# Optimization experiments

Hardware: AMD Instinct MI355X
Metric: run time of the kernel (lower is better)

The kernel has to match this reference:

```python
import jax, jax.numpy as jnp
import numpy as np
from functools import partial

S, E, K = 50000, 20000, 128
B = 16384
NE = 1000000
L = 2  # num_layer


def setup_inputs() -> dict:
    key = jax.random.key(0)
    ks = jax.random.split(key, 24)
    inp = {
        'stu_id': jax.random.randint(ks[0], (B,), 0, S),
        'input_exercise': jax.random.randint(ks[1], (B,), 0, E),
        'input_knowledge_point': jax.random.uniform(ks[2], (B, K), jnp.float32),
        'rows_1': jax.random.randint(ks[3], (NE,), 0, S),
        'cols_1': jax.random.randint(ks[4], (NE,), 0, E),
        'rows_0': jax.random.randint(ks[5], (NE,), 0, S),
        'cols_0': jax.random.randint(ks[6], (NE,), 0, E),
        'vals_ui_1': jax.random.uniform(ks[7], (NE,), jnp.float32),
        'vals_iu_1': jax.random.uniform(ks[8], (NE,), jnp.float32),
        'vals_ui_0': jax.random.uniform(ks[9], (NE,), jnp.float32),
        'vals_iu_0': jax.random.uniform(ks[10], (NE,), jnp.float32),
        'd_i_1': jax.random.uniform(ks[11], (S,), jnp.float32),
        'd_j_1': jax.random.uniform(ks[12], (E,), jnp.float32),
        'd_i_0': jax.random.uniform(ks[13], (S,), jnp.float32),
        'd_j_0': jax.random.uniform(ks[14], (E,), jnp.float32),
        'student_emb': jax.random.normal(ks[15], (S, K), jnp.float32) * 0.1,
        'exercise_emb': jax.random.normal(ks[16], (E, K), jnp.float32) * 0.1,
        'student_emb_bias': jax.random.normal(ks[17], (S, 1), jnp.float32) * 0.1,
        'e_discrimination': jax.random.normal(ks[18], (E, 1), jnp.float32) * 0.1,
        'W1': jax.random.normal(ks[19], (256, K), jnp.float32) * (1.0 / np.sqrt(K)),
        'b1': jnp.zeros((256,), jnp.float32),
        'W2': jax.random.normal(ks[20], (128, 256), jnp.float32) * (1.0 / np.sqrt(256)),
        'b2': jnp.zeros((128,), jnp.float32),
        'W3': jax.random.normal(ks[21], (1, 128), jnp.float32) * (1.0 / np.sqrt(128)),
        'b3': jnp.zeros((1,), jnp.float32),
    }
    return inp


def pos_linear(x, W, b):
    # PosLinear: weight = 2*relu(-W) + W  (== |W|)
    Wp = 2.0 * jax.nn.relu(-W) + W
    return x @ Wp.T + b


def spmm(vals, rows, cols, x, n_out):
    # sparse.mm(A, x) where A has entries vals at (rows, cols); gather cols of x, scatter-add to rows
    return jax.ops.segment_sum(vals[:, None] * x[cols], rows, num_segments=n_out)


def graph_repr(student_emb, exercise_emb,
               rows_1, cols_1, vals_ui_1, vals_iu_1,
               rows_0, cols_0, vals_ui_0, vals_iu_0,
               d_i_1, d_j_1, d_i_0, d_j_0):
    stat = student_emb          # [S, K]
    kdiff = exercise_emb        # [E, K]
    for _ in range(L):
        u1 = spmm(vals_ui_1, rows_1, cols_1, kdiff, S) + stat * d_i_1[:, None]
        i1 = spmm(vals_iu_1, cols_1, rows_1, stat, E) + kdiff * d_j_1[:, None]
        u0 = spmm(vals_ui_0, rows_0, cols_0, kdiff, S) + stat * d_i_0[:, None]
        i0 = spmm(vals_iu_0, cols_0, rows_0, stat, E) + kdiff * d_j_0[:, None]
        stat = u1 + u0
        kdiff = i1 + i0
    return stat, kdiff


def reference(stu_id, input_exercise, input_knowledge_point,
              rows_1, cols_1, rows_0, cols_0,
              vals_ui_1, vals_iu_1, vals_ui_0, vals_iu_0,
              d_i_1, d_j_1, d_i_0, d_j_0,
              student_emb, exercise_emb, student_emb_bias, e_discrimination,
              W1, b1, W2, b2, W3, b3):
    stat, kdiff = graph_repr(student_emb, exercise_emb,
                             rows_1, cols_1, vals_ui_1, vals_iu_1,
                             rows_0, cols_0, vals_ui_0, vals_iu_0,
                             d_i_1, d_j_1, d_i_0, d_j_0)
    e_disc = jax.nn.sigmoid(e_discrimination[input_exercise])          # [B, 1]
    stat_b = jax.nn.sigmoid(stat[stu_id] + student_emb_bias[stu_id])   # [B, K]
    kd = jax.nn.sigmoid(kdiff[input_exercise])                         # [B, K]
    x = input_knowledge_point * (stat_b - kd) * e_disc
    x = jnp.tanh(pos_linear(x, W1, b1))   # dropout is identity in eval
    x = jnp.tanh(pos_linear(x, W2, b2))
    out = jax.nn.sigmoid(pos_linear(x, W3, b3))
    return out.reshape(-1)
```

## Files before the change

### kernel.cpp

```cpp
#include <hip/hip_runtime.h>
#include <hip/hip_fp16.h>

#define S_N 50000
#define E_N 20000
#define K_N 128
#define B_N 16384
#define NE_N 1000000

#define S_PER_XCD 6250
#define E_PER_XCD 2500

#define SCAP 96
#define ECAP 176

#define NBKT 512
#define S_SUB 196
#define E_SUB 79
#define BKCAP 8704
#define OVL_BKTS 257

typedef short bf16x8 __attribute__((ext_vector_type(8)));
typedef float f32x4 __attribute__((ext_vector_type(4)));
typedef int i32x4 __attribute__((ext_vector_type(4)));
typedef float f32x4v __attribute__((ext_vector_type(4)));
typedef unsigned u32x4 __attribute__((ext_vector_type(4)));

__device__ __forceinline__ float sigmoidf_(float v) {
    return 1.0f / (1.0f + __expf(-v));
}
__device__ __forceinline__ float tanh_fast(float v) {
    float e = __expf(2.0f * v);
    return 1.0f - 2.0f / (e + 1.0f);
}
__device__ __forceinline__ unsigned short f2bf(float v) {
    unsigned u = __float_as_uint(v);
    u += 0x7fffu + ((u >> 16) & 1u);
    return (unsigned short)(u >> 16);
}
__device__ __forceinline__ void split_bf(float v, unsigned short& hi, unsigned short& lo) {
    unsigned u = __float_as_uint(v);
    hi = (unsigned short)(u >> 16);
    float fh = __uint_as_float(u & 0xffff0000u);
    lo = f2bf(v - fh);
}
__device__ __forceinline__ float2 h2f2(unsigned u) {
    __half2 h = *(const __half2*)&u;
    return __half22float2(h);
}
__device__ __forceinline__ void accum8(float* acc, uint4 h, float v) {
    float2 p0 = h2f2(h.x);
    float2 p1 = h2f2(h.y);
    float2 p2 = h2f2(h.z);
    float2 p3 = h2f2(h.w);
    acc[0] = fmaf(v, p0.x, acc[0]); acc[1] = fmaf(v, p0.y, acc[1]);
    acc[2] = fmaf(v, p1.x, acc[2]); acc[3] = fmaf(v, p1.y, acc[3]);
    acc[4] = fmaf(v, p2.x, acc[4]); acc[5] = fmaf(v, p2.y, acc[5]);
    acc[6] = fmaf(v, p3.x, acc[6]); acc[7] = fmaf(v, p3.y, acc[7]);
}
__device__ __forceinline__ unsigned f2h2u(float a, float b) {
    __half2 h = __floats2half2_rn(a, b);
    return *(const unsigned*)&h;
}

__device__ __forceinline__ unsigned long long* bslot(
    unsigned long long* ovl, unsigned long long* fr, int b) {
    return (b < OVL_BKTS) ? ovl + (size_t)b * BKCAP
                          : fr + (size_t)(b - OVL_BKTS) * BKCAP;
}

__global__ __launch_bounds__(1024) void bucketize2(
    const i32x4* __restrict__ r1, const i32x4* __restrict__ c1,
    const f32x4v* __restrict__ vui1, const f32x4v* __restrict__ viu1,
    const i32x4* __restrict__ r0, const i32x4* __restrict__ c0,
    const f32x4v* __restrict__ vui0, const f32x4v* __restrict__ viu0,
    unsigned long long* __restrict__ bOvl, unsigned long long* __restrict__ bFr,
    int* __restrict__ gcur) {
    __shared__ int hist[NBKT];
    __shared__ int base[NBKT];
    const int tid = threadIdx.x;
    for (int b = tid; b < NBKT; b += 1024) hist[b] = 0;
    __syncthreads();
    const int NV = NE_N / 4;
    i32x4 rv[2], cv[2]; f32x4v av[2], bv[2];
    int bkt[16], lr[16];
#pragma unroll
    for (int rep = 0; rep < 2; ++rep) {
        int i = blockIdx.x * 2048 + rep * 1024 + tid;
        bool valid = i < 2 * NV;
        if (valid) {
            if (i < NV) {
                rv[rep] = __builtin_nontemporal_load(r1 + i);
                cv[rep] = __builtin_nontemporal_load(c1 + i);
                av[rep] = __builtin_nontemporal_load(vui1 + i);
                bv[rep] = __builtin_nontemporal_load(viu1 + i);
            } else {
                int j = i - NV;
                rv[rep] = __builtin_nontemporal_load(r0 + j);
                cv[rep] = __builtin_nontemporal_load(c0 + j);
                av[rep] = __builtin_nontemporal_load(vui0 + j);
                bv[rep] = __builtin_nontemporal_load(viu0 + j);
            }
        }
#pragma unroll
        for (int k = 0; k < 4; ++k) {
            int u = rep * 8 + k * 2;
            if (valid) {
                int r = rv[rep][k], c = cv[rep][k];
                int xs = r / S_PER_XCD;
                int ss = (r - xs * S_PER_XCD) / S_SUB;
                int xe = c / E_PER_XCD;
                int se = (c - xe * E_PER_XCD) / E_SUB;
                bkt[u] = ss * 8 + xs;
                bkt[u + 1] = 256 + se * 8 + xe;
                lr[u] = atomicAdd(&hist[bkt[u]], 1);
                lr[u + 1] = atomicAdd(&hist[bkt[u + 1]], 1);
            } else {
                bkt[u] = -1; bkt[u + 1] = -1;
            }
        }
    }
    __syncthreads();
    for (int b = tid; b < NBKT; b += 1024) {
        int h = hist[b];
        base[b] = h ? atomicAdd(&gcur[b], h) : 0;
    }
    __syncthreads();
#pragma unroll
    for (int rep = 0; rep < 2; ++rep) {
#pragma unroll
        for (int k = 0; k < 4; ++k) {
            int u = rep * 8 + k * 2;
            if (bkt[u] >= 0) {
                int r = rv[rep][k], c = cv[rep][k];
                unsigned entS = ((unsigned)f2bf(av[rep][k]) << 16) | (unsigned)c;
                unsigned entE = ((unsigned)f2bf(bv[rep][k]) << 16) | (unsigned)r;
                int pS = base[bkt[u]] + lr[u];
                int pE = base[bkt[u + 1]] + lr[u + 1];
                if (pS < BKCAP)
                    bslot(bOvl, bFr, bkt[u])[pS] =
                        ((unsigned long long)(unsigned)r << 32) | entS;
                if (pE < BKCAP)
                    bslot(bOvl, bFr, bkt[u + 1])[pE] =
                        ((unsigned long long)(unsigned)c << 32) | entE;
            }
        }
    }
}

__global__ __launch_bounds__(256) void scatter2(
    unsigned long long* __restrict__ bOvl, unsigned long long* __restrict__ bFr,
    const int* __restrict__ gcur,
    int* __restrict__ cntS, int* __restrict__ cntE,
    unsigned* __restrict__ csrS, unsigned* __restrict__ csrE) {
    __shared__ int lcnt[S_SUB];
    const int bid = blockIdx.x;
    const int tid = threadIdx.x;
    const bool isS = bid < 256;
    const int x = bid & 7;
    const int s = (isS ? bid : bid - 256) >> 3;
    const int start = isS ? x * S_PER_XCD + s * S_SUB : x * E_PER_XCD + s * E_SUB;
    const int len = isS ? min(S_SUB, S_PER_XCD - s * S_SUB)
                        : min(E_SUB, E_PER_XCD - s * E_SUB);
    for (int l = tid; l < len; l += 256) lcnt[l] = 0;
    __syncthreads();
    int n = gcur[bid];
    if (n > BKCAP) n = BKCAP;
    const unsigned long long* bp = bslot(bOvl, bFr, bid);
    for (int i = tid; i < n; i += 256) {
        unsigned long long v = __builtin_nontemporal_load(bp + i);
        int node = (int)(v >> 32);
        unsigned entry = (unsigned)v;
        int slot = atomicAdd(&lcnt[node - start], 1);
        if (isS) {
            if (slot < SCAP) csrS[(size_t)node * SCAP + slot] = entry;
        } else {
            if (slot < ECAP) csrE[(size_t)node * ECAP + slot] = entry;
        }
    }
    __syncthreads();
    for (int l = tid; l < len; l += 256) {
        if (isS) cntS[start + l] = lcnt[l];
        else     cntE[start + l] = lcnt[l];
    }
}

__global__ __launch_bounds__(256) void mark_needed2(
    const int* __restrict__ sid, const int* __restrict__ eid,
    unsigned* __restrict__ maskS, unsigned* __restrict__ maskE) {
    int i = blockIdx.x * blockDim.x + threadIdx.x;
    if (i < B_N) {
        int v = sid[i];
        atomicOr(&maskS[v >> 5], 1u << (v & 31));
    } else if (i < 2 * B_N) {
        int v = eid[i - B_N];
        atomicOr(&maskE[v >> 5], 1u << (v & 31));
    }
}

__global__ __launch_bounds__(256) void cvt_f16_init(
    const float2* __restrict__ sE, const float2* __restrict__ eE,
    __half2* __restrict__ sH, __half2* __restrict__ eH,
    int* __restrict__ cntS, int* __restrict__ cntE,
    unsigned* __restrict__ maskS, unsigned* __restrict__ maskE,
    int* __restrict__ cur) {
    int i = blockIdx.x * 256 + threadIdx.x;
    if (i < S_N) cntS[i] = 0;
    if (i < E_N) cntE[i] = 0;
    if (i < 2048) maskS[i] = 0;
    if (i < 1024) maskE[i] = 0;
    if (i < NBKT) cur[i] = 0;
    const int nS = S_N * 64;
    if (i < nS) {
        float2 v = sE[i];
        sH[i] = __floats2half2_rn(v.x, v.y);
    } else {
        int j = i - nS;
        if (j < E_N * 64) {
            float2 v = eE[j];
            eH[j] = __floats2half2_rn(v.x, v.y);
        }
    }
}

__device__ __forceinline__ void gather_row(
    const uint4* __restrict__ src, const uint4* __restrict__ self,
    const float* __restrict__ dA, const float* __restrict__ dB,
    const int* __restrict__ cnt, const unsigned* __restrict__ csr,
    const unsigned* __restrict__ need,
    uint4* __restrict__ dst, int nrow, int cap, int w, int lane) {
    int slot = lane >> 4;
    int seg = lane & 15;
    if (w >= nrow) return;
    if (need && !((need[w >> 5] >> (w & 31)) & 1u)) return;
    int n = cnt[w];
    if (n > cap) n = cap;
    const unsigned* cbase = csr + (size_t)w * cap;
    float acc[8] = {};
    int i = 0;
    for (; i + 16 <= n; i += 16) {
        unsigned qa = __builtin_nontemporal_load(cbase + i + slot);
        unsigned qb = __builtin_nontemporal_load(cbase + i + 4 + slot);
        unsigned qc = __builtin_nontemporal_load(cbase + i + 8 + slot);
        unsigned qd = __builtin_nontemporal_load(cbase + i + 12 + slot);
        uint4 ha = src[(size_t)(qa & 0xffffu) * 16 + seg];
        uint4 hb = src[(size_t)(qb & 0xffffu) * 16 + seg];
        uint4 hc = src[(size_t)(qc & 0xffffu) * 16 + seg];
        uint4 hd = src[(size_t)(qd & 0xffffu) * 16 + seg];
        accum8(acc, ha, __uint_as_float(qa & 0xffff0000u));
        accum8(acc, hb, __uint_as_float(qb & 0xffff0000u));
        accum8(acc, hc, __uint_as_float(qc & 0xffff0000u));
        accum8(acc, hd, __uint_as_float(qd & 0xffff0000u));
    }
    for (; i + 8 <= n; i += 8) {
        unsigned qa = __builtin_nontemporal_load(cbase + i + slot);
        unsigned qb = __builtin_nontemporal_load(cbase + i + 4 + slot);
        uint4 ha = src[(size_t)(qa & 0xffffu) * 16 + seg];
        uint4 hb = src[(size_t)(qb & 0xffffu) * 16 + seg];
        accum8(acc, ha, __uint_as_float(qa & 0xffff0000u));
        accum8(acc, hb, __uint_as_float(qb & 0xffff0000u));
    }
    for (; i < n; i += 4) {
        int e = i + slot;
        if (e < n) {
            unsigned q = __builtin_nontemporal_load(cbase + e);
            uint4 h = src[(size_t)(q & 0xffffu) * 16 + seg];
            accum8(acc, h, __uint_as_float(q & 0xffff0000u));
        }
    }
#pragma unroll
    for (int j = 0; j < 8; ++j) {
        acc[j] += __shfl_xor(acc[j], 16);
        acc[j] += __shfl_xor(acc[j], 32);
    }
    if (slot == 0) {
        u32x4 hsv = __builtin_nontemporal_load(
            reinterpret_cast<const u32x4*>(self) + ((size_t)w * 16 + seg));
        unsigned h0 = hsv[0], h1 = hsv[1], h2 = hsv[2], h3 = hsv[3];
        float d = dA[w] + dB[w];
        float2 s0 = h2f2(h0);
        float2 s1 = h2f2(h1);
        float2 s2 = h2f2(h2);
        float2 s3 = h2f2(h3);
        u32x4 o;
        o[0] = f2h2u(fmaf(s0.x, d, acc[0]), fmaf(s0.y, d, acc[1]));
        o[1] = f2h2u(fmaf(s1.x, d, acc[2]), fmaf(s1.y, d, acc[3]));
        o[2] = f2h2u(fmaf(s2.x, d, acc[4]), fmaf(s2.y, d, acc[5]));
        o[3] = f2h2u(fmaf(s3.x, d, acc[6]), fmaf(s3.y, d, acc[7]));
        __builtin_nontemporal_store(
            o, reinterpret_cast<u32x4*>(dst) + ((size_t)w * 16 + seg));
    }
}

__global__ __launch_bounds__(256) void gather_dual(
    const uint4* __restrict__ srcE, const uint4* __restrict__ selfE,
    const float* __restrict__ dEA, const float* __restrict__ dEB,
    const int* __restrict__ cntEp, const unsigned* __restrict__ csrEp,
    const unsigned* __restrict__ needE, uint4* __restrict__ dstE,
    const uint4* __restrict__ srcS, const uint4* __restrict__ selfS,
    const float* __restrict__ dSA, const float* __restrict__ dSB,
    const int* __restrict__ cntSp, const unsigned* __restrict__ csrSp,
    const unsigned* __restrict__ needS, uint4* __restrict__ dstS,
    int eBlocks) {
    int lane = threadIdx.x & 63;
    int sub = threadIdx.x >> 6;
    if ((int)blockIdx.x < eBlocks) {
        int w = blockIdx.x * 4 + sub;
        gather_row(srcE, selfE, dEA, dEB, cntEp, csrEp, needE, dstE,
                   E_N, ECAP, w, lane);
    } else {
        int w = (blockIdx.x - eBlocks) * 4 + sub;
        gather_row(srcS, selfS, dSA, dSB, cntSp, csrSp, needS, dstS,
                   S_N, SCAP, w, lane);
    }
}

__global__ __launch_bounds__(256) void feature_abs_kernel(
    const int* __restrict__ stu_id, const int* __restrict__ ex_id,
    const float* __restrict__ ikp,
    const __half2* __restrict__ statH, const __half2* __restrict__ kdiffH,
    const float* __restrict__ s_bias, const float* __restrict__ e_disc,
    unsigned short* __restrict__ xhi, unsigned short* __restrict__ xlo,
    const float* __restrict__ W1, const float* __restrict__ W2,
    unsigned short* __restrict__ w1hi, unsigned short* __restrict__ w1lo,
    unsigned short* __restrict__ w2hi, unsigned short* __restrict__ w2lo,
    int featBlocks) {
    if ((int)blockIdx.x >= featBlocks) {
        int i = (blockIdx.x - featBlocks) * 256 + threadIdx.x;
        unsigned short hi, lo;
        if (i < 32768) {
            split_bf(fabsf(W1[i]), hi, lo);
            w1hi[i] = hi; w1lo[i] = lo;
        } else {
            int j = i - 32768;
            split_bf(fabsf(W2[j]), hi, lo);
            w2hi[j] = hi; w2lo[j] = lo;
        }
        return;
    }
    int i = blockIdx.x * 256 + threadIdx.x;
    int row = i >> 5;
    int k4 = (i & 31) * 4;
    int s = stu_id[row];
    int e = ex_id[row];
    float sb = s_bias[s];
    float ed = sigmoidf_(e_disc[e]);
    float2 s01 = __half22float2(statH[(size_t)s * 64 + (k4 >> 1)]);
    float2 s23 = __half22float2(statH[(size_t)s * 64 + (k4 >> 1) + 1]);
    float2 k01 = __half22float2(kdiffH[(size_t)e * 64 + (k4 >> 1)]);
    float2 k23 = __half22float2(kdiffH[(size_t)e * 64 + (k4 >> 1) + 1]);
    float4 iv = *(const float4*)(ikp + (size_t)row * K_N + k4);
    float f0 = iv.x * (sigmoidf_(s01.x + sb) - sigmoidf_(k01.x)) * ed;
    float f1 = iv.y * (sigmoidf_(s01.y + sb) - sigmoidf_(k01.y)) * ed;
    float f2 = iv.z * (sigmoidf_(s23.x + sb) - sigmoidf_(k23.x)) * ed;
    float f3 = iv.w * (sigmoidf_(s23.y + sb) - sigmoidf_(k23.y)) * ed;
    ushort4 oh, ol;
    split_bf(f0, oh.x, ol.x);
    split_bf(f1, oh.y, ol.y);
    split_bf(f2, oh.z, ol.z);
    split_bf(f3, oh.w, ol.w);
    *(ushort4*)(xhi + (size_t)row * K_N + k4) = oh;
    *(ushort4*)(xlo + (size_t)row * K_N + k4) = ol;
}

#define H1S 264

__global__ __launch_bounds__(256) void mlp_mfma(
    const unsigned short* __restrict__ xhi, const unsigned short* __restrict__ xlo,
    const unsigned short* __restrict__ w1hi, const unsigned short* __restrict__ w1lo,
    const unsigned short* __restrict__ w2hi, const unsigned short* __restrict__ w2lo,
    const float* __restrict__ b1, const float* __restrict__ b2,
    const float* __restrict__ W3, const float* __restrict__ b3,
    float* __restrict__ out) {
    __shared__ unsigned short h1hi[32 * H1S];
    __shared__ unsigned short h1lo[32 * H1S];
    __shared__ float partial[4][32];

    const int t = threadIdx.x;
    const int lane = t & 63;
    const int w = t >> 6;
    const int l15 = lane & 15;
    const int quad = lane >> 4;
    const int r0 = blockIdx.x * 32;

    f32x4 acc1[2][4] = {};
    for (int ks = 0; ks < 128; ks += 32) {
        bf16x8 ah[2], al[2], bh[4], bl[4];
#pragma unroll
        for (int mt = 0; mt < 2; ++mt) {
            size_t o = (size_t)(r0 + mt * 16 + l15) * K_N + ks + quad * 8;
            ah[mt] = *(const bf16x8*)(xhi + o);
            al[mt] = *(const bf16x8*)(xlo + o);
        }
#pragma unroll
        for (int nt = 0; nt < 4; ++nt) {
            size_t o = (size_t)(w * 64 + nt * 16 + l15) * 128 + ks + quad * 8;
            bh[nt] = *(const bf16x8*)(w1hi + o);
            bl[nt] = *(const bf16x8*)(w1lo + o);
        }
#pragma unroll
        for (int mt = 0; mt < 2; ++mt)
#pragma unroll
            for (int nt = 0; nt < 4; ++nt) {
                acc1[mt][nt] = __builtin_amdgcn_mfma_f32_16x16x32_bf16(
                    ah[mt], bh[nt], acc1[mt][nt], 0, 0, 0);
                acc1[mt][nt] = __builtin_amdgcn_mfma_f32_16x16x32_bf16(
                    ah[mt], bl[nt], acc1[mt][nt], 0, 0, 0);
                acc1[mt][nt] = __builtin_amdgcn_mfma_f32_16x16x32_bf16(
                    al[mt], bh[nt], acc1[mt][nt], 0, 0, 0);
            }
    }
#pragma unroll
    for (int nt = 0; nt < 4; ++nt) {
        int c = w * 64 + nt * 16 + l15;
        float bias = b1[c];
#pragma unroll
        for (int mt = 0; mt < 2; ++mt)
#pragma unroll
            for (int rg = 0; rg < 4; ++rg) {
                int row = mt * 16 + quad * 4 + rg;
                float h = tanh_fast(acc1[mt][nt][rg] + bias);
                unsigned short hi, lo;
                split_bf(h, hi, lo);
                h1hi[row * H1S + c] = hi;
                h1lo[row * H1S + c] = lo;
            }
    }
    __syncthreads();

    f32x4 acc2[2][2] = {};
    for (int ks = 0; ks < 256; ks += 32) {
        bf16x8 ah[2], al[2], bh[2], bl[2];
#pragma unroll
        for (int mt = 0; mt < 2; ++mt) {
            int o = (mt * 16 + l15) * H1S + ks + quad * 8;
            ah[mt] = *(const bf16x8*)(&h1hi[o]);
            al[mt] = *(const bf16x8*)(&h1lo[o]);
        }
#pragma unroll
        for (int nt = 0; nt < 2; ++nt) {
            size_t o = (size_t)(w * 32 + nt * 16 + l15) * 256 + ks + quad * 8;
            bh[nt] = *(const bf16x8*)(w2hi + o);
            bl[nt] = *(const bf16x8*)(w2lo + o);
        }
#pragma unroll
        for (int mt = 0; mt < 2; ++mt)
#pragma unroll
            for (int nt = 0; nt < 2; ++nt) {
                acc2[mt][nt] = __builtin_amdgcn_mfma_f32_16x16x32_bf16(
                    ah[mt], bh[nt], acc2[mt][nt], 0, 0, 0);
                acc2[mt][nt] = __builtin_amdgcn_mfma_f32_16x16x32_bf16(
                    ah[mt], bl[nt], acc2[mt][nt], 0, 0, 0);
                acc2[mt][nt] = __builtin_amdgcn_mfma_f32_16x16x32_bf16(
                    al[mt], bh[nt], acc2[mt][nt], 0, 0, 0);
            }
    }

    float w3v[2], b2v[2];
#pragma unroll
    for (int nt = 0; nt < 2; ++nt) {
        int c = w * 32 + nt * 16 + l15;
        w3v[nt] = fabsf(W3[c]);
        b2v[nt] = b2[c];
    }
#pragma unroll
    for (int mt = 0; mt < 2; ++mt)
#pragma unroll
        for (int rg = 0; rg < 4; ++rg) {
            float v = w3v[0] * tanh_fast(acc2[mt][0][rg] + b2v[0]) +
                      w3v[1] * tanh_fast(acc2[mt][1][rg] + b2v[1]);
            v += __shfl_xor(v, 1, 16);
            v += __shfl_xor(v, 2, 16);
            v += __shfl_xor(v, 4, 16);
            v += __shfl_xor(v, 8, 16);
            if (l15 == 0) partial[w][mt * 16 + quad * 4 + rg] = v;
        }
    __syncthreads();
    if (t < 32) {
        float v = partial[0][t] + partial[1][t] + partial[2][t] + partial[3][t];
        out[r0 + t] = sigmoidf_(v + b3[0]);
    }
}

extern "C" void kernel_launch(void* const* d_in, const int* in_sizes, int n_in,
                              void* d_out, int out_size, void* d_ws, size_t ws_size,
                              hipStream_t stream) {
    const int* stu_id        = (const int*)d_in[0];
    const int* input_ex      = (const int*)d_in[1];
    const float* ikp         = (const float*)d_in[2];
    const int* rows_1        = (const int*)d_in[3];
    const int* cols_1        = (const int*)d_in[4];
    const int* rows_0        = (const int*)d_in[5];
    const int* cols_0        = (const int*)d_in[6];
    const float* vals_ui_1   = (const float*)d_in[7];
    const float* vals_iu_1   = (const float*)d_in[8];
    const float* vals_ui_0   = (const float*)d_in[9];
    const float* vals_iu_0   = (const float*)d_in[10];
    const float* d_i_1       = (const float*)d_in[11];
    const float* d_j_1       = (const float*)d_in[12];
    const float* d_i_0       = (const float*)d_in[13];
    const float* d_j_0       = (const float*)d_in[14];
    const float* student_emb = (const float*)d_in[15];
    const float* exercise_emb= (const float*)d_in[16];
    const float* s_bias      = (const float*)d_in[17];
    const float* e_disc      = (const float*)d_in[18];
    const float* W1          = (const float*)d_in[19];
    const float* b1          = (const float*)d_in[20];
    const float* W2          = (const float*)d_in[21];
    const float* b2          = (const float*)d_in[22];
    const float* W3          = (const float*)d_in[23];
    const float* b3          = (const float*)d_in[24];

    char* p = (char*)d_ws;
    __half2* sEH     = (__half2*)p; p += (size_t)S_N * K_N * 2;
    __half2* eEH     = (__half2*)p; p += (size_t)E_N * K_N * 2;
    __half2* statAH  = (__half2*)p; p += (size_t)S_N * K_N * 2;
    __half2* kdiffAH = (__half2*)p; p += (size_t)E_N * K_N * 2;
    unsigned* csrS = (unsigned*)p; p += (size_t)S_N * SCAP * 4;
    unsigned* csrE = (unsigned*)p; p += (size_t)E_N * ECAP * 4;
    int* cntS     = (int*)p;   p += (size_t)S_N * 4;
    int* cntE     = (int*)p;   p += (size_t)E_N * 4;
    unsigned* maskS = (unsigned*)p; p += 2048 * 4;
    unsigned* maskE = (unsigned*)p; p += 1024 * 4;
    int* cur      = (int*)p;   p += NBKT * 4;
    p = (char*)(((size_t)p + 255) & ~(size_t)255);
    unsigned long long* buckFr = (unsigned long long*)p;
    p += (size_t)(NBKT - OVL_BKTS) * BKCAP * 8;
    unsigned long long* buckOvl = (unsigned long long*)statAH;
    __half2* statBH  = sEH;
    __half2* kdiffBH = eEH;
    unsigned short* xhi = (unsigned short*)statAH;
    unsigned short* xlo = xhi + (size_t)B_N * K_N;
    unsigned short* w1hi = (unsigned short*)kdiffAH;
    unsigned short* w1lo = w1hi + 32768;
    unsigned short* w2hi = w1lo + 32768;
    unsigned short* w2lo = w2hi + 32768;

    cvt_f16_init<<<((S_N + E_N) * 64 + 255) / 256, 256, 0, stream>>>(
        (const float2*)student_emb, (const float2*)exercise_emb, sEH, eEH,
        cntS, cntE, maskS, maskE, cur);

    const int bkBlocks = (2 * NE_N / 4 + 2047) / 2048;
    bucketize2<<<bkBlocks, 1024, 0, stream>>>(
        (const i32x4*)rows_1, (const i32x4*)cols_1,
        (const f32x4v*)vals_ui_1, (const f32x4v*)vals_iu_1,
        (const i32x4*)rows_0, (const i32x4*)cols_0,
        (const f32x4v*)vals_ui_0, (const f32x4v*)vals_iu_0,
        buckOvl, buckFr, cur);

    scatter2<<<NBKT, 256, 0, stream>>>(
        buckOvl, buckFr, cur, cntS, cntE, csrS, csrE);

    mark_needed2<<<(2 * B_N + 255) / 256, 256, 0, stream>>>(
        stu_id, input_ex, maskS, maskE);

    const int sGrid = (S_N + 3) / 4;
    const int eGrid = (E_N + 3) / 4;

    gather_dual<<<eGrid + sGrid, 256, 0, stream>>>(
        (const uint4*)sEH, (const uint4*)eEH, d_j_1, d_j_0,
        cntE, csrE, nullptr, (uint4*)kdiffAH,
        (const uint4*)eEH, (const uint4*)sEH, d_i_1, d_i_0,
        cntS, csrS, nullptr, (uint4*)statAH, eGrid);

    gather_dual<<<eGrid + sGrid, 256, 0, stream>>>(
        (const uint4*)statAH, (const uint4*)kdiffAH, d_j_1, d_j_0,
        cntE, csrE, maskE, (uint4*)kdiffBH,
        (const uint4*)kdiffAH, (const uint4*)statAH, d_i_1, d_i_0,
        cntS, csrS, maskS, (uint4*)statBH, eGrid);

    const int featBlocks = B_N * 32 / 256;
    feature_abs_kernel<<<featBlocks + 256, 256, 0, stream>>>(
        stu_id, input_ex, ikp, statBH, kdiffBH, s_bias, e_disc, xhi, xlo,
        W1, W2, w1hi, w1lo, w2hi, w2lo, featBlocks);
    mlp_mfma<<<B_N / 32, 256, 0, stream>>>(xhi, xlo, w1hi, w1lo, w2hi, w2lo,
                                           b1, b2, W3, b3, (float*)d_out);
}
```

Before: 384.8 us.

## Fuse bucket scatter into CSR with first-layer gather per bucket block

Merges the scatter2 kernel and the first gather_dual launch into one scatter_gather kernel. Each 1024-thread block builds the CSR rows for its node range and then immediately aggregates those rows, using the local counts still in shared memory. This removes a launch and lets the freshly written CSR entries be read back while they are likely still in cache. The bucket buffer no longer overlays statAH and gets its own workspace region, so the workspace grows. The fused kernel runs only 512 blocks for the gather work, which may lower parallelism compared with the former wide gather grid.

```diff
diff --git a/kernel.cpp b/kernel.cpp
--- a/kernel.cpp
+++ b/kernel.cpp
@@ -17,7 +17,6 @@
 #define S_SUB 196
 #define E_SUB 79
 #define BKCAP 8704
-#define OVL_BKTS 257
 
 typedef short bf16x8 __attribute__((ext_vector_type(8)));
 typedef float f32x4 __attribute__((ext_vector_type(4)));
@@ -62,19 +61,12 @@
     return *(const unsigned*)&h;
 }
 
-__device__ __forceinline__ unsigned long long* bslot(
-    unsigned long long* ovl, unsigned long long* fr, int b) {
-    return (b < OVL_BKTS) ? ovl + (size_t)b * BKCAP
-                          : fr + (size_t)(b - OVL_BKTS) * BKCAP;
-}
-
 __global__ __launch_bounds__(1024) void bucketize2(
     const i32x4* __restrict__ r1, const i32x4* __restrict__ c1,
     const f32x4v* __restrict__ vui1, const f32x4v* __restrict__ viu1,
     const i32x4* __restrict__ r0, const i32x4* __restrict__ c0,
     const f32x4v* __restrict__ vui0, const f32x4v* __restrict__ viu0,
-    unsigned long long* __restrict__ bOvl, unsigned long long* __restrict__ bFr,
-    int* __restrict__ gcur) {
+    unsigned long long* __restrict__ buck, int* __restrict__ gcur) {
     __shared__ int hist[NBKT];
     __shared__ int base[NBKT];
     const int tid = threadIdx.x;
@@ -137,50 +129,13 @@
                 int pS = base[bkt[u]] + lr[u];
                 int pE = base[bkt[u + 1]] + lr[u + 1];
                 if (pS < BKCAP)
-                    bslot(bOvl, bFr, bkt[u])[pS] =
+                    buck[(size_t)bkt[u] * BKCAP + pS] =
                         ((unsigned long long)(unsigned)r << 32) | entS;
                 if (pE < BKCAP)
-                    bslot(bOvl, bFr, bkt[u + 1])[pE] =
+                    buck[(size_t)bkt[u + 1] * BKCAP + pE] =
                         ((unsigned long long)(unsigned)c << 32) | entE;
             }
         }
-    }
-}
-
-__global__ __launch_bounds__(256) void scatter2(
-    unsigned long long* __restrict__ bOvl, unsigned long long* __restrict__ bFr,
-    const int* __restrict__ gcur,
-    int* __restrict__ cntS, int* __restrict__ cntE,
-    unsigned* __restrict__ csrS, unsigned* __restrict__ csrE) {
-    __shared__ int lcnt[S_SUB];
-    const int bid = blockIdx.x;
-    const int tid = threadIdx.x;
-    const bool isS = bid < 256;
-    const int x = bid & 7;
-    const int s = (isS ? bid : bid - 256) >> 3;
-    const int start = isS ? x * S_PER_XCD + s * S_SUB : x * E_PER_XCD + s * E_SUB;
-    const int len = isS ? min(S_SUB, S_PER_XCD - s * S_SUB)
-                        : min(E_SUB, E_PER_XCD - s * E_SUB);
-    for (int l = tid; l < len; l += 256) lcnt[l] = 0;
-    __syncthreads();
-    int n = gcur[bid];
-    if (n > BKCAP) n = BKCAP;
-    const unsigned long long* bp = bslot(bOvl, bFr, bid);
-    for (int i = tid; i < n; i += 256) {
-        unsigned long long v = __builtin_nontemporal_load(bp + i);
-        int node = (int)(v >> 32);
-        unsigned entry = (unsigned)v;
-        int slot = atomicAdd(&lcnt[node - start], 1);
-        if (isS) {
-            if (slot < SCAP) csrS[(size_t)node * SCAP + slot] = entry;
-        } else {
-            if (slot < ECAP) csrE[(size_t)node * ECAP + slot] = entry;
-        }
-    }
-    __syncthreads();
-    for (int l = tid; l < len; l += 256) {
-        if (isS) cntS[start + l] = lcnt[l];
-        else     cntE[start + l] = lcnt[l];
     }
 }
 
@@ -222,18 +177,13 @@
     }
 }
 
-__device__ __forceinline__ void gather_row(
+__device__ __forceinline__ void gather_row_n(
     const uint4* __restrict__ src, const uint4* __restrict__ self,
     const float* __restrict__ dA, const float* __restrict__ dB,
-    const int* __restrict__ cnt, const unsigned* __restrict__ csr,
-    const unsigned* __restrict__ need,
-    uint4* __restrict__ dst, int nrow, int cap, int w, int lane) {
+    const unsigned* __restrict__ csr,
+    uint4* __restrict__ dst, int cap, int w, int lane, int n) {
     int slot = lane >> 4;
     int seg = lane & 15;
-    if (w >= nrow) return;
-    if (need && !((need[w >> 5] >> (w & 31)) & 1u)) return;
-    int n = cnt[w];
-    if (n > cap) n = cap;
     const unsigned* cbase = csr + (size_t)w * cap;
     float acc[8] = {};
     int i = 0;
@@ -289,6 +239,69 @@
         __builtin_nontemporal_store(
             o, reinterpret_cast<u32x4*>(dst) + ((size_t)w * 16 + seg));
     }
+}
+
+__global__ __launch_bounds__(1024) void scatter_gather(
+    const unsigned long long* __restrict__ buck, const int* __restrict__ gcur,
+    int* __restrict__ cntS, int* __restrict__ cntE,
+    unsigned* __restrict__ csrS, unsigned* __restrict__ csrE,
+    const uint4* __restrict__ sEH, const uint4* __restrict__ eEH,
+    const float* __restrict__ d_i_1, const float* __restrict__ d_i_0,
+    const float* __restrict__ d_j_1, const float* __restrict__ d_j_0,
+    uint4* __restrict__ statAH, uint4* __restrict__ kdiffAH) {
+    __shared__ int lcnt[S_SUB];
+    const int bid = blockIdx.x;
+    const int tid = threadIdx.x;
+    const bool isS = bid < 256;
+    const int x = bid & 7;
+    const int s = (isS ? bid : bid - 256) >> 3;
+    const int start = isS ? x * S_PER_XCD + s * S_SUB : x * E_PER_XCD + s * E_SUB;
+    const int len = isS ? min(S_SUB, S_PER_XCD - s * S_SUB)
+                        : min(E_SUB, E_PER_XCD - s * E_SUB);
+    const int cap = isS ? SCAP : ECAP;
+    unsigned* csr = isS ? csrS : csrE;
+    for (int l = tid; l < len; l += 1024) lcnt[l] = 0;
+    __syncthreads();
+    int n = gcur[bid];
+    if (n > BKCAP) n = BKCAP;
+    const unsigned long long* bp = buck + (size_t)bid * BKCAP;
+    for (int i = tid; i < n; i += 1024) {
+        unsigned long long v = __builtin_nontemporal_load(bp + i);
+        int node = (int)(v >> 32);
+        unsigned entry = (unsigned)v;
+        int slot = atomicAdd(&lcnt[node - start], 1);
+        if (slot < cap) csr[(size_t)node * cap + slot] = entry;
+    }
+    __syncthreads();
+    for (int l = tid; l < len; l += 1024) {
+        int c = min(lcnt[l], cap);
+        if (isS) cntS[start + l] = c;
+        else     cntE[start + l] = c;
+    }
+    const int wave = tid >> 6;
+    const int lane = tid & 63;
+    const uint4* src  = isS ? eEH : sEH;
+    const uint4* self = isS ? sEH : eEH;
+    const float* dA = isS ? d_i_1 : d_j_1;
+    const float* dB = isS ? d_i_0 : d_j_0;
+    uint4* dst = isS ? statAH : kdiffAH;
+    for (int r = wave; r < len; r += 16) {
+        int nn = min(lcnt[r], cap);
+        gather_row_n(src, self, dA, dB, csr, dst, cap, start + r, lane, nn);
+    }
+}
+
+__device__ __forceinline__ void gather_row(
+    const uint4* __restrict__ src, const uint4* __restrict__ self,
+    const float* __restrict__ dA, const float* __restrict__ dB,
+    const int* __restrict__ cnt, const unsigned* __restrict__ csr,
+    const unsigned* __restrict__ need,
+    uint4* __restrict__ dst, int nrow, int cap, int w, int lane) {
+    if (w >= nrow) return;
+    if (need && !((need[w >> 5] >> (w & 31)) & 1u)) return;
+    int n = cnt[w];
+    if (n > cap) n = cap;
+    gather_row_n(src, self, dA, dB, csr, dst, cap, w, lane, n);
 }
 
 __global__ __launch_bounds__(256) void gather_dual(
@@ -523,9 +536,8 @@
     unsigned* maskE = (unsigned*)p; p += 1024 * 4;
     int* cur      = (int*)p;   p += NBKT * 4;
     p = (char*)(((size_t)p + 255) & ~(size_t)255);
-    unsigned long long* buckFr = (unsigned long long*)p;
-    p += (size_t)(NBKT - OVL_BKTS) * BKCAP * 8;
-    unsigned long long* buckOvl = (unsigned long long*)statAH;
+    unsigned long long* buck = (unsigned long long*)p;
+    p += (size_t)NBKT * BKCAP * 8;
     __half2* statBH  = sEH;
     __half2* kdiffBH = eEH;
     unsigned short* xhi = (unsigned short*)statAH;
@@ -545,22 +557,19 @@
         (const f32x4v*)vals_ui_1, (const f32x4v*)vals_iu_1,
         (const i32x4*)rows_0, (const i32x4*)cols_0,
         (const f32x4v*)vals_ui_0, (const f32x4v*)vals_iu_0,
-        buckOvl, buckFr, cur);
-
-    scatter2<<<NBKT, 256, 0, stream>>>(
-        buckOvl, buckFr, cur, cntS, cntE, csrS, csrE);
+        buck, cur);
 
     mark_needed2<<<(2 * B_N + 255) / 256, 256, 0, stream>>>(
         stu_id, input_ex, maskS, maskE);
 
+    scatter_gather<<<NBKT, 1024, 0, stream>>>(
+        buck, cur, cntS, cntE, csrS, csrE,
+        (const uint4*)sEH, (const uint4*)eEH,
+        d_i_1, d_i_0, d_j_1, d_j_0,
+        (uint4*)statAH, (uint4*)kdiffAH);
+
     const int sGrid = (S_N + 3) / 4;
     const int eGrid = (E_N + 3) / 4;
-
-    gather_dual<<<eGrid + sGrid, 256, 0, stream>>>(
-        (const uint4*)sEH, (const uint4*)eEH, d_j_1, d_j_0,
-        cntE, csrE, nullptr, (uint4*)kdiffAH,
-        (const uint4*)eEH, (const uint4*)sEH, d_i_1, d_i_0,
-        cntS, csrS, nullptr, (uint4*)statAH, eGrid);
 
     gather_dual<<<eGrid + sGrid, 256, 0, stream>>>(
         (const uint4*)statAH, (const uint4*)kdiffAH, d_j_1, d_j_0,
```

After: 395.6 us. 2.8% more time.
